# Optimization experiments

Measured on AMD Instinct MI355X. Metric: run time of the kernel, lower is better.

Reference implementation:

```python
import jax, jax.numpy as jnp
import numpy as np

EMBED = 1024
HEADS = 16
HEAD = EMBED // HEADS
B, S = 8, 1024


def setup_inputs() -> dict:
    key = jax.random.key(0)
    ks = jax.random.split(key, 12)
    inp = {
        "values": jax.random.normal(ks[0], (B, S, EMBED), jnp.float32),
        "keys": jax.random.normal(ks[1], (B, S, EMBED), jnp.float32),
        "query": jax.random.normal(ks[2], (B, S, EMBED), jnp.float32),
        # causal mask broadcastable to [B, heads, q, k]
        "mask": jnp.broadcast_to(jnp.tril(jnp.ones((S, S), jnp.int32))[None, None], (B, 1, S, S)),
        "Wv": jax.random.normal(ks[3], (HEAD, HEAD), jnp.float32) / np.sqrt(HEAD),
        "bv": jnp.zeros((HEAD,), jnp.float32),
        "Wk": jax.random.normal(ks[4], (HEAD, HEAD), jnp.float32) / np.sqrt(HEAD),
        "bk": jnp.zeros((HEAD,), jnp.float32),
        "Wq": jax.random.normal(ks[5], (HEAD, HEAD), jnp.float32) / np.sqrt(HEAD),
        "bq": jnp.zeros((HEAD,), jnp.float32),
        "Wfc": jax.random.normal(ks[6], (EMBED, EMBED), jnp.float32) / np.sqrt(EMBED),
        "bfc": jnp.zeros((EMBED,), jnp.float32),
    }
    return inp


def reference(values, keys, query, mask, Wv, bv, Wk, bk, Wq, bq, Wfc, bfc):
    N, q_len = query.shape[0], query.shape[1]
    k_len, v_len = keys.shape[1], values.shape[1]
    # split heads: [N, S, H, D]
    v = values.reshape(N, v_len, HEADS, HEAD)
    k = keys.reshape(N, k_len, HEADS, HEAD)
    q = query.reshape(N, q_len, HEADS, HEAD)
    # per-head linear projections (torch Linear: x @ W.T + b)
    v = v @ Wv.T + bv
    k = k @ Wk.T + bk
    q = q @ Wq.T + bq
    # scores [N, H, q, k]
    scores = jnp.einsum('nqhz,nkhz->nhqk', q, k)
    scores = jnp.where(mask == 0, -jnp.inf, scores)
    # NOTE: original divides by sqrt(query_size) (sequence length), not head dim
    attn = jax.nn.softmax(scores / jnp.sqrt(jnp.float32(q_len)), axis=-1)
    out = jnp.einsum('nhqk,nkhz->nqhz', attn, v).reshape(N, q_len, HEADS * HEAD)
    return out @ Wfc.T + bfc
```

## Files before the change

### kernel.cpp

```cpp
#include <hip/hip_runtime.h>
#include <stdint.h>

typedef __attribute__((ext_vector_type(8))) short short8;
typedef __attribute__((ext_vector_type(4))) short short4v;
typedef __attribute__((ext_vector_type(4))) float floatx4;
typedef __attribute__((ext_vector_type(4))) unsigned short ushort4v;

#define HEADS 16
#define HEAD 64
#define SEQ 1024
#define BATCH 8

__device__ __forceinline__ unsigned short f2bf(float f) {
    union { float f; unsigned int u; } v; v.f = f;
    unsigned int r = v.u + 0x7FFFu + ((v.u >> 16) & 1u);
    return (unsigned short)(r >> 16);
}

__device__ __forceinline__ void gload_lds16(const void* g, void* l) {
    __builtin_amdgcn_global_load_lds((const __attribute__((address_space(1))) void*)g,
                                     (__attribute__((address_space(3))) void*)l, 16, 0, 0);
}

__global__ __launch_bounds__(256) void cvt_kernel(const float* __restrict__ in,
                                                  unsigned short* __restrict__ out) {
    int i = (blockIdx.x * 256 + threadIdx.x) * 4;
    float4 f = *(const float4*)(in + i);
    ushort4v v;
    v.x = f2bf(f.x); v.y = f2bf(f.y); v.z = f2bf(f.z); v.w = f2bf(f.w);
    *(ushort4v*)(out + i) = v;
}

__global__ __launch_bounds__(256) void proj_kernel(
    const float* __restrict__ Vin, const float* __restrict__ Kin, const float* __restrict__ Qin,
    const float* __restrict__ Wv, const float* __restrict__ bv,
    const float* __restrict__ Wk, const float* __restrict__ bk,
    const float* __restrict__ Wq, const float* __restrict__ bq,
    unsigned short* __restrict__ q_ws, unsigned short* __restrict__ k_ws,
    unsigned short* __restrict__ v_ws)
{
    const int tid = threadIdx.x;
    const int tile = blockIdx.x;
    const int ph = blockIdx.y;
    const int proj = ph >> 4;
    const int h = ph & 15;

    const float* X; const float* W; const float* bias;
    if (proj == 0)      { X = Qin; W = Wq; bias = bq; }
    else if (proj == 1) { X = Kin; W = Wk; bias = bk; }
    else                { X = Vin; W = Wv; bias = bv; }

    __shared__ unsigned short sW[64 * 64];
    __shared__ unsigned short sX[64 * 72];

    const int wave = tid >> 6, lane = tid & 63;
    const int lq = lane & 15, quad = lane >> 4;
    const int m0 = tile * 64;

    {
        int n = tid >> 2, c0 = (tid & 3) * 16;
        const float* wr = W + n * 64 + c0;
#pragma unroll
        for (int half = 0; half < 2; ++half) {
            float4 fa = *(const float4*)(wr + half * 8);
            float4 fb = *(const float4*)(wr + half * 8 + 4);
            short8 v;
            v[0] = (short)f2bf(fa.x); v[1] = (short)f2bf(fa.y);
            v[2] = (short)f2bf(fa.z); v[3] = (short)f2bf(fa.w);
            v[4] = (short)f2bf(fb.x); v[5] = (short)f2bf(fb.y);
            v[6] = (short)f2bf(fb.z); v[7] = (short)f2bf(fb.w);
            int chunk = ((c0 >> 3) + half) ^ (n & 7);
            *(short8*)&sW[n * 64 + chunk * 8] = v;
        }
    }

    short8 afr[2];
    {
        const float* xr = X + (size_t)(m0 + wave * 16 + lq) * 1024 + h * 64;
#pragma unroll
        for (int ks = 0; ks < 2; ++ks) {
            float4 f0 = *(const float4*)(xr + quad * 8 + ks * 32);
            float4 f1 = *(const float4*)(xr + quad * 8 + ks * 32 + 4);
            short8 a;
            a[0] = (short)f2bf(f0.x); a[1] = (short)f2bf(f0.y);
            a[2] = (short)f2bf(f0.z); a[3] = (short)f2bf(f0.w);
            a[4] = (short)f2bf(f1.x); a[5] = (short)f2bf(f1.y);
            a[6] = (short)f2bf(f1.z); a[7] = (short)f2bf(f1.w);
            afr[ks] = a;
        }
    }
    __syncthreads();

    const floatx4 zero4 = {0.f, 0.f, 0.f, 0.f};
    floatx4 acc[4] = {zero4, zero4, zero4, zero4};
#pragma unroll
    for (int ks = 0; ks < 2; ++ks) {
#pragma unroll
        for (int nt = 0; nt < 4; ++nt) {
            int n = nt * 16 + lq;
            short8 bfr = *(const short8*)&sW[n * 64 + (((quad + 4 * ks) ^ (n & 7)) * 8)];
            acc[nt] = __builtin_amdgcn_mfma_f32_16x16x32_bf16(afr[ks], bfr, acc[nt], 0, 0, 0);
        }
    }

    const float qscale = 0.03125f * 1.44269504088896340736f;
#pragma unroll
    for (int nt = 0; nt < 4; ++nt) {
        int d = nt * 16 + lq;
        float bcol = bias[d];
#pragma unroll
        for (int r = 0; r < 4; ++r) {
            int srow = wave * 16 + quad * 4 + r;
            float ov = acc[nt][r] + bcol;
            if (proj == 0) ov *= qscale;
            sX[srow * 72 + d] = f2bf(ov);
        }
    }
    __syncthreads();

    const int b = m0 >> 10, s0 = m0 & 1023;
    if (proj < 2) {
        unsigned short* dstb = (proj == 0 ? q_ws : k_ws);
        int r = tid >> 2, c = (tid & 3) * 16;
        unsigned short* dst = dstb + ((size_t)((b * 16 + h) * 1024 + s0 + r)) * 64 + c;
        const unsigned short* src = sX + r * 72 + c;
        ((short4v*)dst)[0] = *(const short4v*)(src);
        ((short4v*)dst)[1] = *(const short4v*)(src + 4);
        ((short4v*)dst)[2] = *(const short4v*)(src + 8);
        ((short4v*)dst)[3] = *(const short4v*)(src + 12);
    } else {
        int d = tid >> 2, c = (tid & 3) * 16;
        short8 v0, v1;
#pragma unroll
        for (int j = 0; j < 8; ++j) v0[j] = (short)sX[(c + j) * 72 + d];
#pragma unroll
        for (int j = 0; j < 8; ++j) v1[j] = (short)sX[(c + 8 + j) * 72 + d];
        unsigned short* dst = v_ws + ((size_t)((b * 16 + h) * 64 + d)) * 1024 + s0 + c;
        *(short8*)dst = v0;
        *(short8*)(dst + 8) = v1;
    }
}

__global__ __launch_bounds__(256, 2) void attn_kernel(
    const unsigned short* __restrict__ q_ws, const unsigned short* __restrict__ k_ws,
    const unsigned short* __restrict__ v_ws, unsigned short* __restrict__ attn_ws)
{
    const int bh = blockIdx.x;
    const int b = bh >> 4, h = bh & 15;
    const int tid = threadIdx.x;
    const int wave = tid >> 6, lane = tid & 63;
    const int lq = lane & 15, quad = lane >> 4;
    const int r8 = lane >> 3, ch = lane & 7;
    const int sw = ch ^ r8;

    __shared__ unsigned short sK[64 * 64];
    __shared__ unsigned short sV[64 * 64];
    __shared__ unsigned short sP[4][32 * 64];

    const size_t head_off = (size_t)bh * SEQ * HEAD;
    const unsigned short* qb = q_ws + head_off;
    const unsigned short* kb = k_ws + head_off;
    const unsigned short* vb = v_ws + head_off;

    short8 ones;
#pragma unroll
    for (int j = 0; j < 8; ++j) ones[j] = (short)0x3F80;

    const floatx4 zero4 = {0.f, 0.f, 0.f, 0.f};

    for (int pass = 0; pass < 2; ++pass) {
        const int qt = pass ? (7 - blockIdx.y) : blockIdx.y;
        const int q0 = qt * 128;
        const int q_lo = q0 + wave * 32;
        const int q_hi = q_lo + 31;
        const int nkt = 2 * qt + 2;

        short8 aq[2][2];
#pragma unroll
        for (int rg = 0; rg < 2; ++rg) {
            const unsigned short* qp = qb + (size_t)(q0 + wave * 32 + rg * 16 + lq) * 64 + quad * 8;
            aq[rg][0] = *(const short8*)qp;
            aq[rg][1] = *(const short8*)(qp + 32);
        }

        floatx4 o[2][4];
        floatx4 lacc[2] = {zero4, zero4};
#pragma unroll
        for (int rg = 0; rg < 2; ++rg)
#pragma unroll
            for (int nt = 0; nt < 4; ++nt) o[rg][nt] = zero4;

        for (int kt = 0; kt < nkt; ++kt) {
#pragma unroll
            for (int i = 0; i < 2; ++i) {
                int br = wave * 16 + i * 8;
                const char* gK = (const char*)(kb + (size_t)(kt * 64 + br + r8) * 64) + sw * 16;
                gload_lds16(gK, (char*)sK + br * 128);
                const char* gV = (const char*)(vb + (size_t)(br + r8) * 1024 + kt * 64) + sw * 16;
                gload_lds16(gV, (char*)sV + br * 128);
            }
            __syncthreads();

            const bool skip = (kt * 64 > q_hi);
            if (!skip) {
                const bool full = (kt * 64 + 63 <= q_lo);

                floatx4 s[2][4];
#pragma unroll
                for (int rg = 0; rg < 2; ++rg)
#pragma unroll
                    for (int nt = 0; nt < 4; ++nt) s[rg][nt] = zero4;
#pragma unroll
                for (int ks = 0; ks < 2; ++ks) {
#pragma unroll
                    for (int nt = 0; nt < 4; ++nt) {
                        short8 kf = *(const short8*)(sK + (nt * 16 + lq) * 64 +
                                                     (((quad + 4 * ks) ^ (lq & 7)) * 8));
                        s[0][nt] = __builtin_amdgcn_mfma_f32_16x16x32_bf16(aq[0][ks], kf, s[0][nt], 0, 0, 0);
                        s[1][nt] = __builtin_amdgcn_mfma_f32_16x16x32_bf16(aq[1][ks], kf, s[1][nt], 0, 0, 0);
                    }
                }

                unsigned short* wp = &sP[wave][0];
#pragma unroll
                for (int rg = 0; rg < 2; ++rg) {
#pragma unroll
                    for (int nt = 0; nt < 4; ++nt) {
                        int kcol = kt * 64 + nt * 16 + lq;
                        int chn = (((nt * 2 + (lq >> 3)) ^ (quad << 1)) * 8) + (lq & 7);
#pragma unroll
                        for (int r = 0; r < 4; ++r) {
                            float p = __builtin_amdgcn_exp2f(s[rg][nt][r]);
                            if (!full) {
                                int qrow = q_lo + rg * 16 + quad * 4 + r;
                                if (kcol > qrow) p = 0.f;
                            }
                            wp[(rg * 16 + quad * 4 + r) * 64 + chn] = f2bf(p);
                        }
                    }
                }

                short8 vf[4][2];
#pragma unroll
                for (int nt = 0; nt < 4; ++nt)
#pragma unroll
                    for (int ks = 0; ks < 2; ++ks)
                        vf[nt][ks] = *(const short8*)(sV + (nt * 16 + lq) * 64 +
                                                      (((quad + 4 * ks) ^ (lq & 7)) * 8));
#pragma unroll
                for (int rg = 0; rg < 2; ++rg) {
#pragma unroll
                    for (int ks = 0; ks < 2; ++ks) {
                        short8 pa = *(const short8*)&sP[wave][(rg * 16 + lq) * 64 +
                                     (((ks * 4 + quad) ^ (((lq >> 2) & 3) << 1)) * 8)];
                        lacc[rg] = __builtin_amdgcn_mfma_f32_16x16x32_bf16(pa, ones, lacc[rg], 0, 0, 0);
#pragma unroll
                        for (int nt = 0; nt < 4; ++nt)
                            o[rg][nt] = __builtin_amdgcn_mfma_f32_16x16x32_bf16(pa, vf[nt][ks], o[rg][nt], 0, 0, 0);
                    }
                }
            }
            __syncthreads();
        }

#pragma unroll
        for (int rg = 0; rg < 2; ++rg) {
            float inv[4];
#pragma unroll
            for (int r = 0; r < 4; ++r) inv[r] = 1.f / lacc[rg][r];
            const int srow_base = q0 + wave * 32 + rg * 16 + quad * 4;
#pragma unroll
            for (int nt = 0; nt < 4; ++nt) {
                int col = h * 64 + nt * 16 + lq;
#pragma unroll
                for (int r = 0; r < 4; ++r) {
                    attn_ws[((size_t)(b * SEQ + srow_base + r)) * 1024 + col] = f2bf(o[rg][nt][r] * inv[r]);
                }
            }
        }
    }
}

__global__ __launch_bounds__(256) void fc_kernel(
    const unsigned short* __restrict__ A, const unsigned short* __restrict__ Bw,
    const float* __restrict__ bias, float* __restrict__ out)
{
    const int nt0 = blockIdx.x * 128;
    const int mt0 = blockIdx.y * 128;
    const int tid = threadIdx.x;
    const int wave = tid >> 6, lane = tid & 63;
    const int lq = lane & 15, quad = lane >> 4;
    const int wm = (wave >> 1) * 64, wn = (wave & 1) * 64;

    __shared__ unsigned short sA[128 * 32];
    __shared__ unsigned short sB[128 * 32];

    const floatx4 zero4 = {0.f, 0.f, 0.f, 0.f};
    floatx4 acc[4][4];
#pragma unroll
    for (int i = 0; i < 4; ++i)
#pragma unroll
        for (int j = 0; j < 4; ++j) acc[i][j] = zero4;

    for (int kt = 0; kt < 32; ++kt) {
#pragma unroll
        for (int issue = 0; issue < 2; ++issue) {
            int off = (issue * 4 + wave) * 1024 + lane * 16;
            int row = off >> 6;
            int cb = off & 63;
            const char* ga = (const char*)A + (size_t)(mt0 + row) * 2048 + kt * 64 + cb;
            gload_lds16(ga, (char*)sA + (issue * 4 + wave) * 1024);
            const char* gb = (const char*)Bw + (size_t)(nt0 + row) * 2048 + kt * 64 + cb;
            gload_lds16(gb, (char*)sB + (issue * 4 + wave) * 1024);
        }
        __syncthreads();

        short8 af[4], bf[4];
#pragma unroll
        for (int i = 0; i < 4; ++i) {
            af[i] = *(const short8*)(sA + (wm + i * 16 + lq) * 32 + quad * 8);
            bf[i] = *(const short8*)(sB + (wn + i * 16 + lq) * 32 + quad * 8);
        }
#pragma unroll
        for (int mi = 0; mi < 4; ++mi)
#pragma unroll
            for (int ni = 0; ni < 4; ++ni)
                acc[mi][ni] = __builtin_amdgcn_mfma_f32_16x16x32_bf16(af[mi], bf[ni], acc[mi][ni], 0, 0, 0);
        __syncthreads();
    }

#pragma unroll
    for (int mi = 0; mi < 4; ++mi) {
#pragma unroll
        for (int ni = 0; ni < 4; ++ni) {
            int col = nt0 + wn + ni * 16 + lq;
            float bc = bias[col];
#pragma unroll
            for (int r = 0; r < 4; ++r) {
                int row = mt0 + wm + mi * 16 + quad * 4 + r;
                out[(size_t)row * 1024 + col] = acc[mi][ni][r] + bc;
            }
        }
    }
}

extern "C" void kernel_launch(void* const* d_in, const int* in_sizes, int n_in,
                              void* d_out, int out_size, void* d_ws, size_t ws_size,
                              hipStream_t stream)
{
    const float* values = (const float*)d_in[0];
    const float* keys   = (const float*)d_in[1];
    const float* query  = (const float*)d_in[2];
    const float* Wv  = (const float*)d_in[4];
    const float* bv  = (const float*)d_in[5];
    const float* Wk  = (const float*)d_in[6];
    const float* bk  = (const float*)d_in[7];
    const float* Wq  = (const float*)d_in[8];
    const float* bq  = (const float*)d_in[9];
    const float* Wfc = (const float*)d_in[10];
    const float* bfc = (const float*)d_in[11];
    float* out = (float*)d_out;

    char* ws = (char*)d_ws;
    unsigned short* q_ws    = (unsigned short*)(ws);
    unsigned short* k_ws    = (unsigned short*)(ws + (16u << 20));
    unsigned short* v_ws    = (unsigned short*)(ws + (32u << 20));
    unsigned short* attn_ws = (unsigned short*)(ws + (48u << 20));
    unsigned short* wfc_ws  = (unsigned short*)(ws + (64u << 20));

    cvt_kernel<<<dim3(1024), dim3(256), 0, stream>>>(Wfc, wfc_ws);
    proj_kernel<<<dim3(128, 48), dim3(256), 0, stream>>>(
        values, keys, query, Wv, bv, Wk, bk, Wq, bq, q_ws, k_ws, v_ws);
    attn_kernel<<<dim3(128, 4), dim3(256), 0, stream>>>(q_ws, k_ws, v_ws, attn_ws);
    fc_kernel<<<dim3(8, 64), dim3(256), 0, stream>>>(attn_ws, wfc_ws, bfc, out);
}
```

Before: 247.0 us.

## Restructure projection kernel to keep weights in registers and loop over heads

The projection kernel drops its LDS staging of the weight matrix and output tile. Each wave now holds the bf16 weight fragments in registers, walks 8 heads per row tile with software-prefetched input loads, and writes outputs straight to global memory. V is computed with swapped MFMA operands so the transposed layout comes out directly. This removes the barriers and per-block weight reloads, but the direct global stores are 2-byte scattered writes, which may coalesce poorly, and the grid is much smaller.

```diff
diff --git a/kernel.cpp b/kernel.cpp
--- a/kernel.cpp
+++ b/kernel.cpp
@@ -40,104 +40,135 @@
     unsigned short* __restrict__ v_ws)
 {
     const int tid = threadIdx.x;
-    const int tile = blockIdx.x;
-    const int ph = blockIdx.y;
-    const int proj = ph >> 4;
-    const int h = ph & 15;
+    const int wave = tid >> 6, lane = tid & 63;
+    const int lq = lane & 15, quad = lane >> 4;
+    const int proj = blockIdx.y;
 
     const float* X; const float* W; const float* bias;
     if (proj == 0)      { X = Qin; W = Wq; bias = bq; }
     else if (proj == 1) { X = Kin; W = Wk; bias = bk; }
     else                { X = Vin; W = Wv; bias = bv; }
 
-    __shared__ unsigned short sW[64 * 64];
-    __shared__ unsigned short sX[64 * 72];
-
-    const int wave = tid >> 6, lane = tid & 63;
-    const int lq = lane & 15, quad = lane >> 4;
-    const int m0 = tile * 64;
-
-    {
-        int n = tid >> 2, c0 = (tid & 3) * 16;
-        const float* wr = W + n * 64 + c0;
-#pragma unroll
-        for (int half = 0; half < 2; ++half) {
-            float4 fa = *(const float4*)(wr + half * 8);
-            float4 fb = *(const float4*)(wr + half * 8 + 4);
+    const int gr0 = blockIdx.x * 32 + (wave & 1) * 16;
+    const int h0 = (wave >> 1) * 8;
+    const int b = gr0 >> 10, s0 = gr0 & 1023;
+
+    short8 wf[4][2];
+#pragma unroll
+    for (int nt = 0; nt < 4; ++nt) {
+        const float* wr = W + (nt * 16 + lq) * 64 + quad * 8;
+#pragma unroll
+        for (int ks = 0; ks < 2; ++ks) {
+            float4 f0 = *(const float4*)(wr + ks * 32);
+            float4 f1 = *(const float4*)(wr + ks * 32 + 4);
             short8 v;
-            v[0] = (short)f2bf(fa.x); v[1] = (short)f2bf(fa.y);
-            v[2] = (short)f2bf(fa.z); v[3] = (short)f2bf(fa.w);
-            v[4] = (short)f2bf(fb.x); v[5] = (short)f2bf(fb.y);
-            v[6] = (short)f2bf(fb.z); v[7] = (short)f2bf(fb.w);
-            int chunk = ((c0 >> 3) + half) ^ (n & 7);
-            *(short8*)&sW[n * 64 + chunk * 8] = v;
+            v[0] = (short)f2bf(f0.x); v[1] = (short)f2bf(f0.y);
+            v[2] = (short)f2bf(f0.z); v[3] = (short)f2bf(f0.w);
+            v[4] = (short)f2bf(f1.x); v[5] = (short)f2bf(f1.y);
+            v[6] = (short)f2bf(f1.z); v[7] = (short)f2bf(f1.w);
+            wf[nt][ks] = v;
         }
     }
 
-    short8 afr[2];
-    {
-        const float* xr = X + (size_t)(m0 + wave * 16 + lq) * 1024 + h * 64;
-#pragma unroll
-        for (int ks = 0; ks < 2; ++ks) {
-            float4 f0 = *(const float4*)(xr + quad * 8 + ks * 32);
-            float4 f1 = *(const float4*)(xr + quad * 8 + ks * 32 + 4);
-            short8 a;
-            a[0] = (short)f2bf(f0.x); a[1] = (short)f2bf(f0.y);
-            a[2] = (short)f2bf(f0.z); a[3] = (short)f2bf(f0.w);
-            a[4] = (short)f2bf(f1.x); a[5] = (short)f2bf(f1.y);
-            a[6] = (short)f2bf(f1.z); a[7] = (short)f2bf(f1.w);
-            afr[ks] = a;
-        }
-    }
-    __syncthreads();
-
+    const float* xb = X + (size_t)(gr0 + lq) * 1024 + quad * 8;
     const floatx4 zero4 = {0.f, 0.f, 0.f, 0.f};
-    floatx4 acc[4] = {zero4, zero4, zero4, zero4};
-#pragma unroll
-    for (int ks = 0; ks < 2; ++ks) {
-#pragma unroll
-        for (int nt = 0; nt < 4; ++nt) {
-            int n = nt * 16 + lq;
-            short8 bfr = *(const short8*)&sW[n * 64 + (((quad + 4 * ks) ^ (n & 7)) * 8)];
-            acc[nt] = __builtin_amdgcn_mfma_f32_16x16x32_bf16(afr[ks], bfr, acc[nt], 0, 0, 0);
-        }
-    }
-
     const float qscale = 0.03125f * 1.44269504088896340736f;
-#pragma unroll
-    for (int nt = 0; nt < 4; ++nt) {
-        int d = nt * 16 + lq;
-        float bcol = bias[d];
-#pragma unroll
-        for (int r = 0; r < 4; ++r) {
-            int srow = wave * 16 + quad * 4 + r;
-            float ov = acc[nt][r] + bcol;
-            if (proj == 0) ov *= qscale;
-            sX[srow * 72 + d] = f2bf(ov);
-        }
-    }
-    __syncthreads();
-
-    const int b = m0 >> 10, s0 = m0 & 1023;
-    if (proj < 2) {
+
+    if (proj == 2) {
+        float bvr[4][4];
+#pragma unroll
+        for (int nt = 0; nt < 4; ++nt)
+#pragma unroll
+            for (int r = 0; r < 4; ++r) bvr[nt][r] = bias[nt * 16 + quad * 4 + r];
+
+        unsigned short* vbp = v_ws + (size_t)(b * 16 + h0) * 64 * 1024 + s0 + lq;
+
+        float4 xf[4];
+        { const float* p = xb + h0 * 64;
+          xf[0] = *(const float4*)p;        xf[1] = *(const float4*)(p + 4);
+          xf[2] = *(const float4*)(p + 32); xf[3] = *(const float4*)(p + 36); }
+#pragma unroll
+        for (int hh = 0; hh < 8; ++hh) {
+            float4 xn[4];
+            if (hh < 7) {
+                const float* p = xb + (h0 + hh + 1) * 64;
+                xn[0] = *(const float4*)p;        xn[1] = *(const float4*)(p + 4);
+                xn[2] = *(const float4*)(p + 32); xn[3] = *(const float4*)(p + 36);
+            }
+            short8 aq[2];
+#pragma unroll
+            for (int ks = 0; ks < 2; ++ks) {
+                short8 a;
+                a[0] = (short)f2bf(xf[ks * 2].x);     a[1] = (short)f2bf(xf[ks * 2].y);
+                a[2] = (short)f2bf(xf[ks * 2].z);     a[3] = (short)f2bf(xf[ks * 2].w);
+                a[4] = (short)f2bf(xf[ks * 2 + 1].x); a[5] = (short)f2bf(xf[ks * 2 + 1].y);
+                a[6] = (short)f2bf(xf[ks * 2 + 1].z); a[7] = (short)f2bf(xf[ks * 2 + 1].w);
+                aq[ks] = a;
+            }
+            floatx4 acc[4] = {zero4, zero4, zero4, zero4};
+#pragma unroll
+            for (int ks = 0; ks < 2; ++ks)
+#pragma unroll
+                for (int nt = 0; nt < 4; ++nt)
+                    acc[nt] = __builtin_amdgcn_mfma_f32_16x16x32_bf16(wf[nt][ks], aq[ks], acc[nt], 0, 0, 0);
+
+            unsigned short* vh = vbp + (size_t)hh * 64 * 1024;
+#pragma unroll
+            for (int nt = 0; nt < 4; ++nt)
+#pragma unroll
+                for (int r = 0; r < 4; ++r)
+                    vh[(size_t)(nt * 16 + quad * 4 + r) * 1024] = f2bf(acc[nt][r] + bvr[nt][r]);
+#pragma unroll
+            for (int i = 0; i < 4; ++i) xf[i] = xn[i];
+        }
+    } else {
+        float bqk[4];
+#pragma unroll
+        for (int nt = 0; nt < 4; ++nt) bqk[nt] = bias[nt * 16 + lq];
+        const float oscale = (proj == 0) ? qscale : 1.0f;
         unsigned short* dstb = (proj == 0 ? q_ws : k_ws);
-        int r = tid >> 2, c = (tid & 3) * 16;
-        unsigned short* dst = dstb + ((size_t)((b * 16 + h) * 1024 + s0 + r)) * 64 + c;
-        const unsigned short* src = sX + r * 72 + c;
-        ((short4v*)dst)[0] = *(const short4v*)(src);
-        ((short4v*)dst)[1] = *(const short4v*)(src + 4);
-        ((short4v*)dst)[2] = *(const short4v*)(src + 8);
-        ((short4v*)dst)[3] = *(const short4v*)(src + 12);
-    } else {
-        int d = tid >> 2, c = (tid & 3) * 16;
-        short8 v0, v1;
-#pragma unroll
-        for (int j = 0; j < 8; ++j) v0[j] = (short)sX[(c + j) * 72 + d];
-#pragma unroll
-        for (int j = 0; j < 8; ++j) v1[j] = (short)sX[(c + 8 + j) * 72 + d];
-        unsigned short* dst = v_ws + ((size_t)((b * 16 + h) * 64 + d)) * 1024 + s0 + c;
-        *(short8*)dst = v0;
-        *(short8*)(dst + 8) = v1;
+        unsigned short* qkp = dstb + ((size_t)((b * 16 + h0) * 1024) + s0 + quad * 4) * 64 + lq;
+
+        float4 xf[4];
+        { const float* p = xb + h0 * 64;
+          xf[0] = *(const float4*)p;        xf[1] = *(const float4*)(p + 4);
+          xf[2] = *(const float4*)(p + 32); xf[3] = *(const float4*)(p + 36); }
+#pragma unroll
+        for (int hh = 0; hh < 8; ++hh) {
+            float4 xn[4];
+            if (hh < 7) {
+                const float* p = xb + (h0 + hh + 1) * 64;
+                xn[0] = *(const float4*)p;        xn[1] = *(const float4*)(p + 4);
+                xn[2] = *(const float4*)(p + 32); xn[3] = *(const float4*)(p + 36);
+            }
+            short8 aq[2];
+#pragma unroll
+            for (int ks = 0; ks < 2; ++ks) {
+                short8 a;
+                a[0] = (short)f2bf(xf[ks * 2].x);     a[1] = (short)f2bf(xf[ks * 2].y);
+                a[2] = (short)f2bf(xf[ks * 2].z);     a[3] = (short)f2bf(xf[ks * 2].w);
+                a[4] = (short)f2bf(xf[ks * 2 + 1].x); a[5] = (short)f2bf(xf[ks * 2 + 1].y);
+                a[6] = (short)f2bf(xf[ks * 2 + 1].z); a[7] = (short)f2bf(xf[ks * 2 + 1].w);
+                aq[ks] = a;
+            }
+            floatx4 acc[4] = {zero4, zero4, zero4, zero4};
+#pragma unroll
+            for (int ks = 0; ks < 2; ++ks)
+#pragma unroll
+                for (int nt = 0; nt < 4; ++nt)
+                    acc[nt] = __builtin_amdgcn_mfma_f32_16x16x32_bf16(aq[ks], wf[nt][ks], acc[nt], 0, 0, 0);
+
+            unsigned short* qh = qkp + (size_t)hh * 1024 * 64;
+#pragma unroll
+            for (int nt = 0; nt < 4; ++nt)
+#pragma unroll
+                for (int r = 0; r < 4; ++r) {
+                    float ov = (acc[nt][r] + bqk[nt]) * oscale;
+                    qh[r * 64 + nt * 16] = f2bf(ov);
+                }
+#pragma unroll
+            for (int i = 0; i < 4; ++i) xf[i] = xn[i];
+        }
     }
 }
 
@@ -369,7 +400,7 @@
     unsigned short* wfc_ws  = (unsigned short*)(ws + (64u << 20));
 
     cvt_kernel<<<dim3(1024), dim3(256), 0, stream>>>(Wfc, wfc_ws);
-    proj_kernel<<<dim3(128, 48), dim3(256), 0, stream>>>(
+    proj_kernel<<<dim3(256, 3), dim3(256), 0, stream>>>(
         values, keys, query, Wv, bv, Wk, bk, Wq, bq, q_ws, k_ws, v_ws);
     attn_kernel<<<dim3(128, 4), dim3(256), 0, stream>>>(q_ws, k_ws, v_ws, attn_ws);
     fc_kernel<<<dim3(8, 64), dim3(256), 0, stream>>>(attn_ws, wfc_ws, bfc, out);
```

After: 253.7 us. 2.7% more time.
